# Performance work log

Hardware: AMD Instinct MI355X
Metric: run time of the kernel (lower is better)

The kernel has to match this reference:

```python
import jax, jax.numpy as jnp
import numpy as np

K = 2  # inputs per LUT

def _codes(k, kk, dtype):
    # [kk, k] matrix of +/-1 sign codes enumerating the 2^k binary corners
    bits = ((np.arange(kk)[:, None] >> np.arange(k)[None, :]) & 1).astype(np.float32)
    return jnp.asarray(bits * 2.0 - 1.0, dtype=dtype)

def setup_inputs() -> dict:
    key = jax.random.key(0)
    k1, k2, k3, k4 = jax.random.split(key, 4)
    B, IN, OUT = 64, 512, 512
    T = IN * OUT                      # tables_count
    KK = 2 ** K
    input = jax.random.normal(k1, (B, IN), dtype=jnp.float32)
    input_mask = jax.random.randint(k2, (T * K,), 0, IN, dtype=jnp.int32)
    lut_weights = jax.random.normal(k3, (T, KK), dtype=jnp.float32)
    bias = jax.random.normal(k4, (OUT,), dtype=jnp.float32) * 0.05
    return {"input": input, "input_mask": input_mask,
            "lut_weights": lut_weights, "bias": bias}

def reference(input, input_mask, lut_weights, bias):
    B = input.shape[0]
    T, KK = lut_weights.shape
    OUT = bias.shape[0]
    # irregular gather: expanded_input = input[:, input_mask] -> [B, T, K]
    x = jnp.take(input, input_mask, axis=1).reshape(B, T, K)
    codes = _codes(K, KK, input.dtype)           # [KK, K]
    # Lagrange interpolation over hypercube corners: prod_j (1 + s_j x_j)/2
    acc = jnp.ones((B, T, KK), dtype=input.dtype)
    for j in range(K):                           # k is tiny and static
        acc = acc * ((1.0 + codes[:, j] * x[:, :, j:j + 1]) * 0.5)
    per_table = jnp.einsum('btc,tc->bt', acc, lut_weights)  # [B, T]
    # segment-sum tables -> out_features (tables contiguous per out_feature)
    out = per_table.reshape(B, OUT, T // OUT).sum(-1) + bias
    return out
```

## Files before the change

### kernel.cpp

```cpp
#include <hip/hip_runtime.h>

constexpr int B    = 64;
constexpr int IN   = 512;
constexpr int OUT  = 512;
constexpr int T    = IN * OUT;
constexpr int TPO  = T / OUT;
constexpr int STRB = 144;

__device__ __forceinline__ unsigned short f2bf(float x) {
    unsigned u = __float_as_uint(x);
    return (unsigned short)((u + 0x7FFFu + ((u >> 16) & 1u)) >> 16);
}
__device__ __forceinline__ float bf_lo(unsigned u) { return __uint_as_float(u << 16); }
__device__ __forceinline__ float bf_hi(unsigned u) { return __uint_as_float(u & 0xFFFF0000u); }

__global__ __launch_bounds__(1024, 8)
void lut_main_kernel(const float* __restrict__ input,
                     const int2*  __restrict__ mask2,
                     const float4* __restrict__ lut,
                     const float* __restrict__ bias,
                     float* __restrict__ out) {
    __shared__ unsigned int xs_u[IN * STRB / 4];
    __shared__ float red[16 * B];

    const int tid = threadIdx.x;
    const int o   = blockIdx.x;

    {
        const int i = tid & (IN - 1);
        const int h = tid >> 9;
        char* rowp = (char*)xs_u + i * STRB + h * 64;
#pragma unroll
        for (int q = 0; q < 4; ++q) {
            const int b0 = 32 * h + 8 * q;
            float a0 = input[(b0 + 0) * IN + i], a1 = input[(b0 + 1) * IN + i];
            float a2 = input[(b0 + 2) * IN + i], a3 = input[(b0 + 3) * IN + i];
            float a4 = input[(b0 + 4) * IN + i], a5 = input[(b0 + 5) * IN + i];
            float a6 = input[(b0 + 6) * IN + i], a7 = input[(b0 + 7) * IN + i];
            uint4 pk;
            pk.x = (unsigned)f2bf(a0) | ((unsigned)f2bf(a1) << 16);
            pk.y = (unsigned)f2bf(a2) | ((unsigned)f2bf(a3) << 16);
            pk.z = (unsigned)f2bf(a4) | ((unsigned)f2bf(a5) << 16);
            pk.w = (unsigned)f2bf(a6) | ((unsigned)f2bf(a7) << 16);
            *reinterpret_cast<uint4*>(rowp + 16 * q) = pk;
        }
    }
    __syncthreads();

    const int lane = tid & 63;
    const int w    = tid >> 6;
    const int tg   = lane >> 3;
    const int bo   = lane & 7;
    const int t0   = o * TPO + w * 32;

    const float4 ca = lut[t0 + (lane & 31)];
    float sA = (ca.x + ca.y + ca.z + ca.w) * 0.25f;
#pragma unroll
    for (int s = 1; s < 32; s <<= 1) sA += __shfl_xor(sA, s);

    const char* xb = (const char*)xs_u + 16 * bo;
    float acc[8] = {0, 0, 0, 0, 0, 0, 0, 0};

#pragma unroll
    for (int s = 0; s < 4; ++s) {
        const int    t = t0 + 8 * s + tg;
        const int2   m = mask2[t];
        const float4 c = lut[t];
        const float Bc = (-c.x + c.y - c.z + c.w) * 0.25f;
        const float Cc = (-c.x - c.y + c.z + c.w) * 0.25f;
        const float Dd = ( c.x - c.y - c.z + c.w) * 0.25f;
        const uint4 u0 = *reinterpret_cast<const uint4*>(xb + m.x * STRB);
        const uint4 u1 = *reinterpret_cast<const uint4*>(xb + m.y * STRB);
        const unsigned p0[4] = {u0.x, u0.y, u0.z, u0.w};
        const unsigned p1[4] = {u1.x, u1.y, u1.z, u1.w};
#pragma unroll
        for (int e = 0; e < 4; ++e) {
            const float x0l = bf_lo(p0[e]), x0h = bf_hi(p0[e]);
            const float x1l = bf_lo(p1[e]), x1h = bf_hi(p1[e]);
            acc[2 * e]     = fmaf(Bc, x0l, fmaf(Cc, x1l,
                              fmaf(Dd, x0l * x1l, acc[2 * e])));
            acc[2 * e + 1] = fmaf(Bc, x0h, fmaf(Cc, x1h,
                              fmaf(Dd, x0h * x1h, acc[2 * e + 1])));
        }
    }

#pragma unroll
    for (int mask = 8; mask <= 32; mask <<= 1) {
#pragma unroll
        for (int e = 0; e < 8; ++e) acc[e] += __shfl_xor(acc[e], mask);
    }
    if (tg == 0) {
#pragma unroll
        for (int e = 0; e < 8; ++e)
            red[w * B + 8 * bo + e] = acc[e] + sA;
    }
    __syncthreads();

    if (tid < B) {
        float s = 0.f;
#pragma unroll
        for (int q = 0; q < 16; ++q) s += red[q * B + tid];
        out[tid * OUT + o] = s + bias[o];
    }
}

extern "C" void kernel_launch(void* const* d_in, const int* in_sizes, int n_in,
                              void* d_out, int out_size, void* d_ws, size_t ws_size,
                              hipStream_t stream) {
    const float*  input = (const float*)d_in[0];
    const int*    mask  = (const int*)d_in[1];
    const float*  lut   = (const float*)d_in[2];
    const float*  bias  = (const float*)d_in[3];
    float*        out   = (float*)d_out;

    dim3 grid(OUT), block(1024);
    lut_main_kernel<<<grid, block, 0, stream>>>(
        input, (const int2*)mask, (const float4*)lut, bias, out);
}
```

Baseline: 13.95 us.

## Split into prep kernel that precomputes packed records and bf16 input rows

Adds a prep kernel that converts the input to a bf16 row layout once in workspace, and packs each table's mask indices and interpolation coefficients into a 16-byte record. It also folds the constant term into a per-output bias. The main kernel then copies the prepacked rows straight into shared memory and reads one record per table. This removes the repeated strided input conversion in every block and the redundant coefficient arithmetic, at the cost of a second launch and extra workspace traffic. The 16-bit index packing relies on IN fitting in 16 bits.

```diff
diff --git a/kernel.cpp b/kernel.cpp
--- a/kernel.cpp
+++ b/kernel.cpp
@@ -6,44 +6,83 @@
 constexpr int T    = IN * OUT;
 constexpr int TPO  = T / OUT;
 constexpr int STRB = 144;
+constexpr int XCH  = IN * STRB / 16;
 
-__device__ __forceinline__ unsigned short f2bf(float x) {
+constexpr size_t REC_OFF  = 0;
+constexpr size_t X_OFF    = (size_t)T * 16;
+constexpr size_t BIAS_OFF = X_OFF + 80 * 1024;
+
+__device__ __forceinline__ unsigned f2bf(float x) {
     unsigned u = __float_as_uint(x);
-    return (unsigned short)((u + 0x7FFFu + ((u >> 16) & 1u)) >> 16);
+    return (u + 0x7FFFu + ((u >> 16) & 1u)) >> 16;
 }
 __device__ __forceinline__ float bf_lo(unsigned u) { return __uint_as_float(u << 16); }
 __device__ __forceinline__ float bf_hi(unsigned u) { return __uint_as_float(u & 0xFFFF0000u); }
 
+__global__ __launch_bounds__(256)
+void prep_kernel(const float* __restrict__ input, const int2* __restrict__ mask2,
+                 const float4* __restrict__ lut, const float* __restrict__ bias,
+                 unsigned char* __restrict__ ws) {
+    __shared__ float ps[4];
+    const int tid = threadIdx.x;
+    if (blockIdx.x < OUT) {
+        const int o = blockIdx.x;
+        uint4* rec = reinterpret_cast<uint4*>(ws + REC_OFF);
+        float sA = 0.f;
+#pragma unroll
+        for (int h = 0; h < 2; ++h) {
+            const int t = o * TPO + h * 256 + tid;
+            const int2   m = mask2[t];
+            const float4 c = lut[t];
+            sA += ( c.x + c.y + c.z + c.w) * 0.25f;
+            const float Bc = (-c.x + c.y - c.z + c.w) * 0.25f;
+            const float Cc = (-c.x - c.y + c.z + c.w) * 0.25f;
+            const float Dd = ( c.x - c.y - c.z + c.w) * 0.25f;
+            uint4 r;
+            r.x = (unsigned)(m.x | (m.y << 16));
+            r.y = __float_as_uint(Bc);
+            r.z = __float_as_uint(Cc);
+            r.w = __float_as_uint(Dd);
+            rec[t] = r;
+        }
+#pragma unroll
+        for (int s = 1; s < 64; s <<= 1) sA += __shfl_xor(sA, s);
+        if ((tid & 63) == 0) ps[tid >> 6] = sA;
+        __syncthreads();
+        if (tid == 0) {
+            float* bias2 = reinterpret_cast<float*>(ws + BIAS_OFF);
+            bias2[o] = bias[o] + ps[0] + ps[1] + ps[2] + ps[3];
+        }
+    } else {
+        const int i = (blockIdx.x - OUT) * 256 + tid;
+        unsigned pk[32];
+#pragma unroll
+        for (int k = 0; k < 32; ++k) {
+            const float a0 = input[(2 * k    ) * IN + i];
+            const float a1 = input[(2 * k + 1) * IN + i];
+            pk[k] = f2bf(a0) | (f2bf(a1) << 16);
+        }
+        uint4* row = reinterpret_cast<uint4*>(ws + X_OFF + (size_t)i * STRB);
+#pragma unroll
+        for (int q = 0; q < 8; ++q)
+            row[q] = make_uint4(pk[4*q], pk[4*q+1], pk[4*q+2], pk[4*q+3]);
+    }
+}
+
 __global__ __launch_bounds__(1024, 8)
-void lut_main_kernel(const float* __restrict__ input,
-                     const int2*  __restrict__ mask2,
-                     const float4* __restrict__ lut,
-                     const float* __restrict__ bias,
+void lut_main_kernel(const unsigned char* __restrict__ ws,
                      float* __restrict__ out) {
-    __shared__ unsigned int xs_u[IN * STRB / 4];
+    __shared__ uint4 xs4[XCH];
     __shared__ float red[16 * B];
 
     const int tid = threadIdx.x;
     const int o   = blockIdx.x;
 
-    {
-        const int i = tid & (IN - 1);
-        const int h = tid >> 9;
-        char* rowp = (char*)xs_u + i * STRB + h * 64;
+    const uint4* wx = reinterpret_cast<const uint4*>(ws + X_OFF);
 #pragma unroll
-        for (int q = 0; q < 4; ++q) {
-            const int b0 = 32 * h + 8 * q;
-            float a0 = input[(b0 + 0) * IN + i], a1 = input[(b0 + 1) * IN + i];
-            float a2 = input[(b0 + 2) * IN + i], a3 = input[(b0 + 3) * IN + i];
-            float a4 = input[(b0 + 4) * IN + i], a5 = input[(b0 + 5) * IN + i];
-            float a6 = input[(b0 + 6) * IN + i], a7 = input[(b0 + 7) * IN + i];
-            uint4 pk;
-            pk.x = (unsigned)f2bf(a0) | ((unsigned)f2bf(a1) << 16);
-            pk.y = (unsigned)f2bf(a2) | ((unsigned)f2bf(a3) << 16);
-            pk.z = (unsigned)f2bf(a4) | ((unsigned)f2bf(a5) << 16);
-            pk.w = (unsigned)f2bf(a6) | ((unsigned)f2bf(a7) << 16);
-            *reinterpret_cast<uint4*>(rowp + 16 * q) = pk;
-        }
+    for (int c = 0; c < 5; ++c) {
+        const int idx = tid + c * 1024;
+        if (idx < XCH) xs4[idx] = wx[idx];
     }
     __syncthreads();
 
@@ -53,46 +92,39 @@
     const int bo   = lane & 7;
     const int t0   = o * TPO + w * 32;
 
-    const float4 ca = lut[t0 + (lane & 31)];
-    float sA = (ca.x + ca.y + ca.z + ca.w) * 0.25f;
-#pragma unroll
-    for (int s = 1; s < 32; s <<= 1) sA += __shfl_xor(sA, s);
+    const uint4* rec = reinterpret_cast<const uint4*>(ws + REC_OFF) + t0 + tg;
+    const char*  xb  = reinterpret_cast<const char*>(xs4) + 16 * bo;
 
-    const char* xb = (const char*)xs_u + 16 * bo;
     float acc[8] = {0, 0, 0, 0, 0, 0, 0, 0};
-
 #pragma unroll
     for (int s = 0; s < 4; ++s) {
-        const int    t = t0 + 8 * s + tg;
-        const int2   m = mask2[t];
-        const float4 c = lut[t];
-        const float Bc = (-c.x + c.y - c.z + c.w) * 0.25f;
-        const float Cc = (-c.x - c.y + c.z + c.w) * 0.25f;
-        const float Dd = ( c.x - c.y - c.z + c.w) * 0.25f;
-        const uint4 u0 = *reinterpret_cast<const uint4*>(xb + m.x * STRB);
-        const uint4 u1 = *reinterpret_cast<const uint4*>(xb + m.y * STRB);
+        const uint4 r  = rec[8 * s];
+        const float Bc = __uint_as_float(r.y);
+        const float Cc = __uint_as_float(r.z);
+        const float Dd = __uint_as_float(r.w);
+        const int   i0 = r.x & 0xFFFF;
+        const int   i1 = r.x >> 16;
+        const uint4 u0 = *reinterpret_cast<const uint4*>(xb + i0 * STRB);
+        const uint4 u1 = *reinterpret_cast<const uint4*>(xb + i1 * STRB);
         const unsigned p0[4] = {u0.x, u0.y, u0.z, u0.w};
         const unsigned p1[4] = {u1.x, u1.y, u1.z, u1.w};
 #pragma unroll
         for (int e = 0; e < 4; ++e) {
             const float x0l = bf_lo(p0[e]), x0h = bf_hi(p0[e]);
             const float x1l = bf_lo(p1[e]), x1h = bf_hi(p1[e]);
-            acc[2 * e]     = fmaf(Bc, x0l, fmaf(Cc, x1l,
-                              fmaf(Dd, x0l * x1l, acc[2 * e])));
-            acc[2 * e + 1] = fmaf(Bc, x0h, fmaf(Cc, x1h,
-                              fmaf(Dd, x0h * x1h, acc[2 * e + 1])));
+            acc[2*e]   = fmaf(Bc, x0l, fmaf(Cc, x1l, fmaf(Dd, x0l * x1l, acc[2*e])));
+            acc[2*e+1] = fmaf(Bc, x0h, fmaf(Cc, x1h, fmaf(Dd, x0h * x1h, acc[2*e+1])));
         }
     }
 
 #pragma unroll
-    for (int mask = 8; mask <= 32; mask <<= 1) {
+    for (int m = 8; m <= 32; m <<= 1) {
 #pragma unroll
-        for (int e = 0; e < 8; ++e) acc[e] += __shfl_xor(acc[e], mask);
+        for (int e = 0; e < 8; ++e) acc[e] += __shfl_xor(acc[e], m);
     }
     if (tg == 0) {
 #pragma unroll
-        for (int e = 0; e < 8; ++e)
-            red[w * B + 8 * bo + e] = acc[e] + sA;
+        for (int e = 0; e < 8; ++e) red[w * B + 8 * bo + e] = acc[e];
     }
     __syncthreads();
 
@@ -100,20 +132,22 @@
         float s = 0.f;
 #pragma unroll
         for (int q = 0; q < 16; ++q) s += red[q * B + tid];
-        out[tid * OUT + o] = s + bias[o];
+        const float* bias2 = reinterpret_cast<const float*>(ws + BIAS_OFF);
+        out[tid * OUT + o] = s + bias2[o];
     }
 }
 
 extern "C" void kernel_launch(void* const* d_in, const int* in_sizes, int n_in,
                               void* d_out, int out_size, void* d_ws, size_t ws_size,
                               hipStream_t stream) {
-    const float*  input = (const float*)d_in[0];
-    const int*    mask  = (const int*)d_in[1];
-    const float*  lut   = (const float*)d_in[2];
-    const float*  bias  = (const float*)d_in[3];
-    float*        out   = (float*)d_out;
+    const float* input = (const float*)d_in[0];
+    const int*   mask  = (const int*)d_in[1];
+    const float* lut   = (const float*)d_in[2];
+    const float* bias  = (const float*)d_in[3];
+    float*       out   = (float*)d_out;
+    unsigned char* ws  = (unsigned char*)d_ws;
 
-    dim3 grid(OUT), block(1024);
-    lut_main_kernel<<<grid, block, 0, stream>>>(
-        input, (const int2*)mask, (const float4*)lut, bias, out);
+    prep_kernel<<<dim3(OUT + 2), dim3(256), 0, stream>>>(
+        input, (const int2*)mask, (const float4*)lut, bias, ws);
+    lut_main_kernel<<<dim3(OUT), dim3(1024), 0, stream>>>(ws, out);
 }
```

Result: slower. 28.52 us (+104.5%).

## Split batch across two blocks per output to halve shared staging and double grid

Applied to the files above, without the earlier changes.

The grid gains a second dimension that splits the 64-row batch into two halves of 32, so each block stages only 32 bf16 batch columns per input row (80-byte stride) in shared memory. Lanes are remapped so each lane handles 8 batch elements of a quarter-batch and two tables, with mask/LUT loads hoisted before the compute loop. The intent is to cut per-block LDS staging work and footprint and to double the block count for better occupancy and latency hiding. In exchange, every table's mask and LUT entry is read by two blocks, and the whole input matrix is staged twice overall.

```diff
diff --git a/kernel.cpp b/kernel.cpp
--- a/kernel.cpp
+++ b/kernel.cpp
@@ -5,11 +5,12 @@
 constexpr int OUT  = 512;
 constexpr int T    = IN * OUT;
 constexpr int TPO  = T / OUT;
-constexpr int STRB = 144;
+constexpr int BH   = 32;
+constexpr int ROWB = 80;
 
-__device__ __forceinline__ unsigned short f2bf(float x) {
+__device__ __forceinline__ unsigned f2bf(float x) {
     unsigned u = __float_as_uint(x);
-    return (unsigned short)((u + 0x7FFFu + ((u >> 16) & 1u)) >> 16);
+    return (u + 0x7FFFu + ((u >> 16) & 1u)) >> 16;
 }
 __device__ __forceinline__ float bf_lo(unsigned u) { return __uint_as_float(u << 16); }
 __device__ __forceinline__ float bf_hi(unsigned u) { return __uint_as_float(u & 0xFFFF0000u); }
@@ -20,100 +21,99 @@
                      const float4* __restrict__ lut,
                      const float* __restrict__ bias,
                      float* __restrict__ out) {
-    __shared__ unsigned int xs_u[IN * STRB / 4];
-    __shared__ float red[16 * B];
+    __shared__ unsigned char xs[IN * ROWB];
+    __shared__ float red[16 * BH];
 
     const int tid = threadIdx.x;
     const int o   = blockIdx.x;
+    const int h   = blockIdx.y;
 
     {
-        const int i = tid & (IN - 1);
-        const int h = tid >> 9;
-        char* rowp = (char*)xs_u + i * STRB + h * 64;
+        const int i     = tid & (IN - 1);
+        const int hh    = tid >> 9;
+        const int bbase = h * BH + hh * 16;
+        unsigned pk[8];
 #pragma unroll
-        for (int q = 0; q < 4; ++q) {
-            const int b0 = 32 * h + 8 * q;
-            float a0 = input[(b0 + 0) * IN + i], a1 = input[(b0 + 1) * IN + i];
-            float a2 = input[(b0 + 2) * IN + i], a3 = input[(b0 + 3) * IN + i];
-            float a4 = input[(b0 + 4) * IN + i], a5 = input[(b0 + 5) * IN + i];
-            float a6 = input[(b0 + 6) * IN + i], a7 = input[(b0 + 7) * IN + i];
-            uint4 pk;
-            pk.x = (unsigned)f2bf(a0) | ((unsigned)f2bf(a1) << 16);
-            pk.y = (unsigned)f2bf(a2) | ((unsigned)f2bf(a3) << 16);
-            pk.z = (unsigned)f2bf(a4) | ((unsigned)f2bf(a5) << 16);
-            pk.w = (unsigned)f2bf(a6) | ((unsigned)f2bf(a7) << 16);
-            *reinterpret_cast<uint4*>(rowp + 16 * q) = pk;
+        for (int j = 0; j < 8; ++j) {
+            const float a0 = input[(bbase + 2 * j    ) * IN + i];
+            const float a1 = input[(bbase + 2 * j + 1) * IN + i];
+            pk[j] = f2bf(a0) | (f2bf(a1) << 16);
         }
+        uint4* dst = reinterpret_cast<uint4*>(xs + i * ROWB + hh * 32);
+        dst[0] = make_uint4(pk[0], pk[1], pk[2], pk[3]);
+        dst[1] = make_uint4(pk[4], pk[5], pk[6], pk[7]);
     }
     __syncthreads();
 
     const int lane = tid & 63;
     const int w    = tid >> 6;
-    const int tg   = lane >> 3;
-    const int bo   = lane & 7;
     const int t0   = o * TPO + w * 32;
+    const int tg   = lane >> 2;
+    const int bq   = lane & 3;
 
     const float4 ca = lut[t0 + (lane & 31)];
     float sA = (ca.x + ca.y + ca.z + ca.w) * 0.25f;
 #pragma unroll
     for (int s = 1; s < 32; s <<= 1) sA += __shfl_xor(sA, s);
 
-    const char* xb = (const char*)xs_u + 16 * bo;
+    const int2   m0 = mask2[t0 + tg];
+    const int2   m1 = mask2[t0 + 16 + tg];
+    const float4 c0 = lut[t0 + tg];
+    const float4 c1 = lut[t0 + 16 + tg];
+
+    const unsigned char* xb = xs + 16 * bq;
     float acc[8] = {0, 0, 0, 0, 0, 0, 0, 0};
 
 #pragma unroll
-    for (int s = 0; s < 4; ++s) {
-        const int    t = t0 + 8 * s + tg;
-        const int2   m = mask2[t];
-        const float4 c = lut[t];
+    for (int s = 0; s < 2; ++s) {
+        const int2   m = s ? m1 : m0;
+        const float4 c = s ? c1 : c0;
         const float Bc = (-c.x + c.y - c.z + c.w) * 0.25f;
         const float Cc = (-c.x - c.y + c.z + c.w) * 0.25f;
         const float Dd = ( c.x - c.y - c.z + c.w) * 0.25f;
-        const uint4 u0 = *reinterpret_cast<const uint4*>(xb + m.x * STRB);
-        const uint4 u1 = *reinterpret_cast<const uint4*>(xb + m.y * STRB);
+        const uint4 u0 = *reinterpret_cast<const uint4*>(xb + m.x * ROWB);
+        const uint4 u1 = *reinterpret_cast<const uint4*>(xb + m.y * ROWB);
         const unsigned p0[4] = {u0.x, u0.y, u0.z, u0.w};
         const unsigned p1[4] = {u1.x, u1.y, u1.z, u1.w};
 #pragma unroll
         for (int e = 0; e < 4; ++e) {
             const float x0l = bf_lo(p0[e]), x0h = bf_hi(p0[e]);
             const float x1l = bf_lo(p1[e]), x1h = bf_hi(p1[e]);
-            acc[2 * e]     = fmaf(Bc, x0l, fmaf(Cc, x1l,
-                              fmaf(Dd, x0l * x1l, acc[2 * e])));
-            acc[2 * e + 1] = fmaf(Bc, x0h, fmaf(Cc, x1h,
-                              fmaf(Dd, x0h * x1h, acc[2 * e + 1])));
+            acc[2*e]   = fmaf(Bc, x0l, fmaf(Cc, x1l, fmaf(Dd, x0l * x1l, acc[2*e])));
+            acc[2*e+1] = fmaf(Bc, x0h, fmaf(Cc, x1h, fmaf(Dd, x0h * x1h, acc[2*e+1])));
         }
     }
 
 #pragma unroll
-    for (int mask = 8; mask <= 32; mask <<= 1) {
+    for (int msk = 4; msk <= 32; msk <<= 1) {
 #pragma unroll
-        for (int e = 0; e < 8; ++e) acc[e] += __shfl_xor(acc[e], mask);
+        for (int e = 0; e < 8; ++e) acc[e] += __shfl_xor(acc[e], msk);
     }
     if (tg == 0) {
 #pragma unroll
         for (int e = 0; e < 8; ++e)
-            red[w * B + 8 * bo + e] = acc[e] + sA;
+            red[w * BH + 8 * bq + e] = acc[e] + sA;
     }
     __syncthreads();
 
-    if (tid < B) {
+    if (tid < BH) {
         float s = 0.f;
 #pragma unroll
-        for (int q = 0; q < 16; ++q) s += red[q * B + tid];
-        out[tid * OUT + o] = s + bias[o];
+        for (int q = 0; q < 16; ++q) s += red[q * BH + tid];
+        out[(h * BH + tid) * OUT + o] = s + bias[o];
     }
 }
 
 extern "C" void kernel_launch(void* const* d_in, const int* in_sizes, int n_in,
                               void* d_out, int out_size, void* d_ws, size_t ws_size,
                               hipStream_t stream) {
-    const float*  input = (const float*)d_in[0];
-    const int*    mask  = (const int*)d_in[1];
-    const float*  lut   = (const float*)d_in[2];
-    const float*  bias  = (const float*)d_in[3];
-    float*        out   = (float*)d_out;
+    const float* input = (const float*)d_in[0];
+    const int*   mask  = (const int*)d_in[1];
+    const float* lut   = (const float*)d_in[2];
+    const float* bias  = (const float*)d_in[3];
+    float*       out   = (float*)d_out;
 
-    dim3 grid(OUT), block(1024);
+    dim3 grid(OUT, 2), block(1024);
     lut_main_kernel<<<grid, block, 0, stream>>>(
         input, (const int2*)mask, (const float4*)lut, bias, out);
 }
```

Result: slower. 16.48 us (+18.2%).
